# Kernel tuning notes

Measured on AMD Instinct MI355X. Metric: run time of the kernel, lower is better.

The kernel has to match this reference:

```python
import jax, jax.numpy as jnp
import numpy as np

V = 100000
E = 1600000
B, FIN, K, FOUT = 2, 32, 4, 32


def setup_inputs() -> dict:
    key = jax.random.key(0)
    k1, k2, k3, k4, k5, k6 = jax.random.split(key, 6)
    inputs = jax.random.normal(k1, (B, V, FIN), dtype=jnp.float32)
    lap_rows = jax.random.randint(k2, (E,), 0, V, dtype=jnp.int32)
    lap_cols = jax.random.randint(k3, (E,), 0, V, dtype=jnp.int32)
    # scale values so the Chebyshev recursion stays numerically tame
    lap_vals = jax.random.normal(k4, (E,), dtype=jnp.float32) * 0.1
    weight = jax.random.normal(k5, (FIN, K, FOUT), dtype=jnp.float32) * 0.05
    bias = jax.random.normal(k6, (FOUT,), dtype=jnp.float32)
    return {"inputs": inputs, "lap_rows": lap_rows, "lap_cols": lap_cols,
            "lap_vals": lap_vals, "weight": weight, "bias": bias}


def _spmm(rows, cols, vals, x):
    # sparse [V,V] @ dense [B,V,F] -> [B,V,F]
    gathered = jnp.take(x, cols, axis=1)            # [B,E,F]
    contrib = vals[None, :, None] * gathered        # [B,E,F]
    out = jax.ops.segment_sum(contrib.swapaxes(0, 1), rows, num_segments=V)  # [V,B,F]
    return out.swapaxes(0, 1)


def reference(inputs, lap_rows, lap_cols, lap_vals, weight, bias):
    k = weight.shape[1]
    x0 = inputs
    terms = [x0]
    if k > 1:
        x1 = _spmm(lap_rows, lap_cols, lap_vals, x0)
        terms.append(x1)
    for _ in range(2, k):
        x2 = 2.0 * _spmm(lap_rows, lap_cols, lap_vals, x1) - x0
        terms.append(x2)
        x0, x1 = x1, x2
    x = jnp.stack(terms, axis=-1)                   # [B,V,Fin,K]
    out = jnp.einsum('bvfk,fko->bvo', x, weight) + bias
    return out
```

## Files before the change

### kernel.cpp

```cpp
#include <hip/hip_runtime.h>
#include <hip/hip_bf16.h>

#define NV 100000
#define NE 1600000
#define NB 2
#define FIN 32
#define NK 4
#define FOUT 32

#define RPB 128
#define NBUCK ((NV + RPB - 1) / RPB)
#define SLAB 2816
#define CHUNK 8192
#define GCHUNK ((NE + CHUNK - 1) / CHUNK)
#define GCONV (((long)NV * 64 + 1023) / 1024)

typedef long long ll;


__global__ void scale_init_kernel(float* __restrict__ dst, const float* __restrict__ src,
                                  float alpha, int n) {
    int i = blockIdx.x * blockDim.x + threadIdx.x;
    if (i < n) dst[i] = alpha * src[i];
}

__global__ void spmm_scatter_kernel(float* __restrict__ y, const float* __restrict__ x,
                                    const int* __restrict__ rows, const int* __restrict__ cols,
                                    const float* __restrict__ vals, float scale) {
    long tid = (long)blockIdx.x * blockDim.x + threadIdx.x;
    int e = (int)(tid >> 5);
    int f = (int)(tid & 31);
    if (e >= NE) return;
    int r = rows[e];
    int c = cols[e];
    float v = scale * vals[e];
#pragma unroll
    for (int b = 0; b < NB; ++b) {
        float g = x[(long)b * NV * FIN + (long)c * FIN + f];
        atomicAdd(&y[(long)b * NV * FIN + (long)r * FIN + f], v * g);
    }
}

__global__ void term_gemm_kernel(float* __restrict__ out, const float* __restrict__ x,
                                 const float* __restrict__ weight, const float* __restrict__ bias,
                                 int k, int first) {
    __shared__ float Wl[FIN][FOUT];
    __shared__ float Xl[8][FIN];
    int tid = threadIdx.x;
    for (int i = tid; i < FIN * FOUT; i += 256) {
        int f = i >> 5, o = i & 31;
        Wl[f][o] = weight[f * (NK * FOUT) + k * FOUT + o];
    }
    long rbase = (long)blockIdx.x * 8;
    for (int i = tid; i < 8 * FIN; i += 256) {
        int rv = i >> 5, f = i & 31;
        Xl[rv][f] = x[(rbase + rv) * FIN + f];
    }
    __syncthreads();
    int rv = tid >> 5, o = tid & 31;
    float acc = 0.f;
#pragma unroll
    for (int f = 0; f < FIN; ++f) acc += Xl[rv][f] * Wl[f][o];
    long r = rbase + rv;
    if (first) out[r * FOUT + o] = acc + bias[o];
    else       out[r * FOUT + o] += acc;
}

__global__ __launch_bounds__(1024)
void convert_place_kernel(const int* __restrict__ rows, const int* __restrict__ cols,
                          const float* __restrict__ vals, int* __restrict__ gcursor,
                          ll* __restrict__ edges,
                          __hip_bfloat16* __restrict__ xb, const float* __restrict__ inputs) {
    if (blockIdx.x >= GCHUNK) {
        long i = (long)(blockIdx.x - GCHUNK) * 1024 + threadIdx.x;
        if (i < (long)NV * 64) {
            int lane = (int)(i & 63);
            long v = i >> 6;
            int b = lane >> 5, f = lane & 31;
            xb[i] = __float2bfloat16(inputs[(long)b * NV * FIN + v * FIN + f]);
        }
        return;
    }
    __shared__ int cnt[NBUCK];
    __shared__ int cur[NBUCK];
    for (int i = threadIdx.x; i < NBUCK; i += 1024) cnt[i] = 0;
    __syncthreads();
    long base = (long)blockIdx.x * CHUNK;
    int lim = (base + CHUNK <= NE) ? CHUNK : (int)(NE - base);
    for (int i = threadIdx.x; i < lim; i += 1024)
        atomicAdd(&cnt[rows[base + i] >> 7], 1);
    __syncthreads();
    for (int i = threadIdx.x; i < NBUCK; i += 1024)
        cur[i] = cnt[i] ? (i * SLAB + atomicAdd(&gcursor[i], cnt[i])) : 0;
    __syncthreads();
    if (lim == CHUNK) {
        int bb[8]; ll rec[8]; int pos[8];
#pragma unroll
        for (int u = 0; u < 8; ++u) {
            int i = threadIdx.x + u * 1024;
            int r = rows[base + i];
            bb[u] = r >> 7;
            unsigned int lo = ((unsigned int)cols[base + i]) | (((unsigned int)(r & 127)) << 17);
            unsigned int hi = __float_as_uint(vals[base + i]);
            rec[u] = (ll)lo | ((ll)hi << 32);
        }
#pragma unroll
        for (int u = 0; u < 8; ++u) pos[u] = atomicAdd(&cur[bb[u]], 1);
#pragma unroll
        for (int u = 0; u < 8; ++u)
            if (pos[u] < (bb[u] + 1) * SLAB) edges[pos[u]] = rec[u];
    } else {
        for (int i = threadIdx.x; i < lim; i += 1024) {
            int r = rows[base + i];
            int b = r >> 7;
            unsigned int lo = ((unsigned int)cols[base + i]) | (((unsigned int)(r & 127)) << 17);
            unsigned int hi = __float_as_uint(vals[base + i]);
            int pos = atomicAdd(&cur[b], 1);
            if (pos < (b + 1) * SLAB) edges[pos] = (ll)lo | ((ll)hi << 32);
        }
    }
}

__global__ __launch_bounds__(512)
void bucket_sort_kernel(ll* __restrict__ edges, const int* __restrict__ gcursor,
                        int* __restrict__ row_start, int* __restrict__ counts) {
    __shared__ ll recL[SLAB];
    __shared__ int rcnt[RPB];
    __shared__ int pcnt[RPB];
    __shared__ int rcur[RPB];
    __shared__ int ssc[RPB];
    int b = blockIdx.x;
    int base = b * SLAB;
    int n = gcursor[b];
    if (n > SLAB) n = SLAB;
    if (n < 0) n = 0;
    int t = threadIdx.x;
    if (t < RPB) rcnt[t] = 0;
    __syncthreads();
    {
        ll rc[4]; int lr[4]; bool vld[4];
#pragma unroll
        for (int u = 0; u < 4; ++u) {
            int i = t + u * 512;
            vld[u] = (i < n);
            if (vld[u]) { rc[u] = edges[base + i]; recL[i] = rc[u]; lr[u] = (int)((rc[u] >> 17) & 127); }
        }
#pragma unroll
        for (int u = 0; u < 4; ++u) if (vld[u]) atomicAdd(&rcnt[lr[u]], 1);
        for (int i = t + 2048; i < n; i += 512) {
            ll rec = edges[base + i];
            recL[i] = rec;
            atomicAdd(&rcnt[(int)((rec >> 17) & 127)], 1);
        }
    }
    __syncthreads();
    if (t < RPB) pcnt[t] = (rcnt[t] + 7) & ~7;
    __syncthreads();
    if (t < RPB) ssc[t] = pcnt[t];
    __syncthreads();
    for (int off = 1; off < RPB; off <<= 1) {
        int x = 0;
        if (t < RPB && t >= off) x = ssc[t - off];
        __syncthreads();
        if (t < RPB) ssc[t] += x;
        __syncthreads();
    }
    if (ssc[RPB - 1] > SLAB) {
        __syncthreads();
        if (t < RPB) { pcnt[t] = rcnt[t]; ssc[t] = rcnt[t]; }
        __syncthreads();
        for (int off = 1; off < RPB; off <<= 1) {
            int x = 0;
            if (t < RPB && t >= off) x = ssc[t - off];
            __syncthreads();
            if (t < RPB) ssc[t] += x;
            __syncthreads();
        }
    }
    __syncthreads();
    if (t < RPB) {
        int ex = ssc[t] - pcnt[t];
        rcur[t] = ex;
        int v = b * RPB + t;
        if (v < NV) { row_start[v] = base + ex; counts[v] = pcnt[t]; }
    }
    __syncthreads();
    {
        ll rc[4]; int lr[4]; int pos[4]; bool vld[4];
#pragma unroll
        for (int u = 0; u < 4; ++u) {
            int i = t + u * 512;
            vld[u] = (i < n);
            if (vld[u]) { rc[u] = recL[i]; lr[u] = (int)((rc[u] >> 17) & 127); }
        }
#pragma unroll
        for (int u = 0; u < 4; ++u) if (vld[u]) pos[u] = atomicAdd(&rcur[lr[u]], 1);
#pragma unroll
        for (int u = 0; u < 4; ++u) if (vld[u]) edges[base + pos[u]] = rc[u];
        for (int i = t + 2048; i < n; i += 512) {
            ll rec = recL[i];
            int pos = atomicAdd(&rcur[(int)((rec >> 17) & 127)], 1);
            edges[base + pos] = rec;
        }
    }
    __syncthreads();
    if (t < RPB) {
        int start = ssc[t] - pcnt[t];
        for (int i = rcnt[t]; i < pcnt[t]; ++i)
            edges[base + start + i] = 0;
    }
}

__global__ __launch_bounds__(256)
void spmm_gather_kernel(__hip_bfloat16* __restrict__ xnext, const __hip_bfloat16* __restrict__ xcur,
                        const __hip_bfloat16* __restrict__ xprev,
                        const int* __restrict__ row_start, const int* __restrict__ counts,
                        const ll* __restrict__ edges, float alpha, float beta) {
    int r = blockIdx.x * (blockDim.x >> 6) + (threadIdx.x >> 6);
    int lane = threadIdx.x & 63;
    int s = __builtin_amdgcn_readfirstlane(row_start[r]);
    int cnt = __builtin_amdgcn_readfirstlane(counts[r]);
    const ll* ep = edges + s;
    float acc = 0.f;
    int j = 0;
    for (; j + 16 <= cnt; j += 16) {
        ll e[16];
        unsigned int g[16];
#pragma unroll
        for (int u = 0; u < 16; ++u) e[u] = ep[j + u];
#pragma unroll
        for (int u = 0; u < 16; ++u)
            g[u] = ((const unsigned short*)xcur)[(long)(e[u] & 0x1FFFF) * 64 + lane];
#pragma unroll
        for (int u = 0; u < 16; ++u)
            acc = fmaf(__uint_as_float((unsigned int)((unsigned long long)e[u] >> 32)),
                       __uint_as_float((unsigned int)g[u] << 16), acc);
    }
    if (j + 8 <= cnt) {
        ll e[8];
        unsigned int g[8];
#pragma unroll
        for (int u = 0; u < 8; ++u) e[u] = ep[j + u];
#pragma unroll
        for (int u = 0; u < 8; ++u)
            g[u] = ((const unsigned short*)xcur)[(long)(e[u] & 0x1FFFF) * 64 + lane];
#pragma unroll
        for (int u = 0; u < 8; ++u)
            acc = fmaf(__uint_as_float((unsigned int)((unsigned long long)e[u] >> 32)),
                       __uint_as_float((unsigned int)g[u] << 16), acc);
        j += 8;
    }
    for (; j < cnt; ++j) {
        ll e0 = ep[j];
        unsigned int g0 = ((const unsigned short*)xcur)[(long)(e0 & 0x1FFFF) * 64 + lane];
        acc = fmaf(__uint_as_float((unsigned int)((unsigned long long)e0 >> 32)),
                   __uint_as_float(g0 << 16), acc);
    }
    long o = (long)r * 64 + lane;
    float res = alpha * acc;
    if (beta != 0.f) res += beta * __bfloat162float(xprev[o]);
    xnext[o] = __float2bfloat16(res);
}

__global__ __launch_bounds__(256)
void final_gemm_kernel(float* __restrict__ out,
                       const __hip_bfloat16* __restrict__ xb0,
                       const __hip_bfloat16* __restrict__ xb1,
                       const __hip_bfloat16* __restrict__ xb2,
                       const __hip_bfloat16* __restrict__ xb3,
                       const float* __restrict__ weight,
                       const float* __restrict__ bias) {
    int t = blockIdx.x * blockDim.x + threadIdx.x;
    if (t >= NV * NB) return;
    int oh = blockIdx.y * 16;
    int v = t >> 1, b = t & 1;
    float acc[16];
#pragma unroll
    for (int o = 0; o < 16; ++o) acc[o] = bias[oh + o];
    for (int k = 0; k < NK; ++k) {
        const __hip_bfloat16* xr = (k == 0) ? xb0 : (k == 1) ? xb1 : (k == 2) ? xb2 : xb3;
        const uint4* xp = (const uint4*)(xr + (long)v * 64 + b * 32);
        uint4 q0 = xp[0], q1 = xp[1], q2 = xp[2], q3 = xp[3];
        unsigned int qq[16] = {q0.x, q0.y, q0.z, q0.w, q1.x, q1.y, q1.z, q1.w,
                               q2.x, q2.y, q2.z, q2.w, q3.x, q3.y, q3.z, q3.w};
        const float* wk = weight + k * FOUT + oh;
#pragma unroll
        for (int i = 0; i < 16; ++i) {
            float xlo = __uint_as_float(qq[i] << 16);
            float xhi = __uint_as_float(qq[i] & 0xffff0000u);
            const float* w0 = wk + (2 * i) * (NK * FOUT);
            const float* w1 = wk + (2 * i + 1) * (NK * FOUT);
#pragma unroll
            for (int o = 0; o < 16; ++o) {
                acc[o] = fmaf(xlo, w0[o], acc[o]);
                acc[o] = fmaf(xhi, w1[o], acc[o]);
            }
        }
    }
    float* op = out + (long)b * NV * FOUT + (long)v * FOUT + oh;
#pragma unroll
    for (int o = 0; o < 16; ++o) op[o] = acc[o];
}

extern "C" void kernel_launch(void* const* d_in, const int* in_sizes, int n_in,
                              void* d_out, int out_size, void* d_ws, size_t ws_size,
                              hipStream_t stream) {
    const float* inputs = (const float*)d_in[0];
    const int*   rows   = (const int*)d_in[1];
    const int*   cols   = (const int*)d_in[2];
    const float* vals   = (const float*)d_in[3];
    const float* weight = (const float*)d_in[4];
    const float* bias   = (const float*)d_in[5];
    float* out = (float*)d_out;

    const long n = (long)NB * NV * FIN;
    const int gG = (NB * NV) / 8;
    const int gRow = NV / 4;
    const int gGemm = (NV * NB + 255) / 256;
    const int gFused = GCHUNK + (int)GCONV;

    int* gcursor   = (int*)d_ws;
    int* row_start = gcursor + 1024;
    int* counts    = row_start + NV;
    ll* edges      = (ll*)(counts + NV);
    size_t off = (size_t)((char*)(edges + (long)NBUCK * SLAB) - (char*)d_ws);
    off = (off + 255) & ~(size_t)255;
    __hip_bfloat16* xb0 = (__hip_bfloat16*)((char*)d_ws + off);
    __hip_bfloat16* xb1 = xb0 + (long)NV * 64;
    __hip_bfloat16* xb2 = xb1 + (long)NV * 64;
    __hip_bfloat16* xb3 = xb2 + (long)NV * 64;
    size_t need = off + 4 * (size_t)NV * 64 * sizeof(__hip_bfloat16);

    if (ws_size < need) {
        float* fA = (float*)d_ws;
        float* fB = fA + n;
        const int gNf = (int)((n + 255) / 256);
        const int gEf = (NE * 32 + 255) / 256;
        term_gemm_kernel<<<gG, 256, 0, stream>>>(out, inputs, weight, bias, 0, 1);
        scale_init_kernel<<<gNf, 256, 0, stream>>>(fA, inputs, 0.f, (int)n);
        spmm_scatter_kernel<<<gEf, 256, 0, stream>>>(fA, inputs, rows, cols, vals, 1.f);
        term_gemm_kernel<<<gG, 256, 0, stream>>>(out, fA, weight, bias, 1, 0);
        scale_init_kernel<<<gNf, 256, 0, stream>>>(fB, inputs, -1.f, (int)n);
        spmm_scatter_kernel<<<gEf, 256, 0, stream>>>(fB, fA, rows, cols, vals, 2.f);
        term_gemm_kernel<<<gG, 256, 0, stream>>>(out, fB, weight, bias, 2, 0);
        scale_init_kernel<<<gNf, 256, 0, stream>>>(fA, fA, -1.f, (int)n);
        spmm_scatter_kernel<<<gEf, 256, 0, stream>>>(fA, fB, rows, cols, vals, 2.f);
        term_gemm_kernel<<<gG, 256, 0, stream>>>(out, fA, weight, bias, 3, 0);
        return;
    }

    hipMemsetAsync(gcursor, 0, (size_t)NBUCK * sizeof(int), stream);
    convert_place_kernel<<<gFused, 1024, 0, stream>>>(rows, cols, vals, gcursor, edges,
                                                      xb0, inputs);
    bucket_sort_kernel<<<NBUCK, 512, 0, stream>>>(edges, gcursor, row_start, counts);

    spmm_gather_kernel<<<gRow, 256, 0, stream>>>(xb1, xb0, nullptr, row_start, counts,
                                                 edges, 1.f, 0.f);
    spmm_gather_kernel<<<gRow, 256, 0, stream>>>(xb2, xb1, xb0, row_start, counts,
                                                 edges, 2.f, -1.f);
    spmm_gather_kernel<<<gRow, 256, 0, stream>>>(xb3, xb2, xb1, row_start, counts,
                                                 edges, 2.f, -1.f);

    final_gemm_kernel<<<dim3(gGemm, 2), 256, 0, stream>>>(out, xb0, xb1, xb2, xb3,
                                                          weight, bias);
}
```

Measured before the change: 183.2 us.

## Fuse first SpMM gather into bucket sort kernel using LDS-resident sorted edges

The bucket sort kernel now keeps the row-sorted edge records in a second shared-memory array and, after sorting, computes the first Chebyshev SpMM (x1 = L x0) for its own 128 rows directly from LDS. The separate first spmm_gather launch goes away, along with its global reads of the edge list, row_start and counts. In exchange, LDS use per block doubles (two 2816-entry 64-bit arrays), which may lower occupancy. The gather runs with only 8 waves per block over 128 rows, so it has less latency hiding than the standalone kernel.

```diff
diff --git a/kernel.cpp b/kernel.cpp
--- a/kernel.cpp
+++ b/kernel.cpp
@@ -122,9 +122,12 @@
 }
 
 __global__ __launch_bounds__(512)
-void bucket_sort_kernel(ll* __restrict__ edges, const int* __restrict__ gcursor,
-                        int* __restrict__ row_start, int* __restrict__ counts) {
+void sort_gather_kernel(ll* __restrict__ edges, const int* __restrict__ gcursor,
+                        int* __restrict__ row_start, int* __restrict__ counts,
+                        __hip_bfloat16* __restrict__ xnext,
+                        const __hip_bfloat16* __restrict__ xcur) {
     __shared__ ll recL[SLAB];
+    __shared__ ll recS[SLAB];
     __shared__ int rcnt[RPB];
     __shared__ int pcnt[RPB];
     __shared__ int rcur[RPB];
@@ -196,18 +199,65 @@
 #pragma unroll
         for (int u = 0; u < 4; ++u) if (vld[u]) pos[u] = atomicAdd(&rcur[lr[u]], 1);
 #pragma unroll
-        for (int u = 0; u < 4; ++u) if (vld[u]) edges[base + pos[u]] = rc[u];
+        for (int u = 0; u < 4; ++u)
+            if (vld[u]) { recS[pos[u]] = rc[u]; edges[base + pos[u]] = rc[u]; }
         for (int i = t + 2048; i < n; i += 512) {
             ll rec = recL[i];
             int pos = atomicAdd(&rcur[(int)((rec >> 17) & 127)], 1);
+            recS[pos] = rec;
             edges[base + pos] = rec;
         }
     }
     __syncthreads();
     if (t < RPB) {
         int start = ssc[t] - pcnt[t];
-        for (int i = rcnt[t]; i < pcnt[t]; ++i)
+        for (int i = rcnt[t]; i < pcnt[t]; ++i) {
+            recS[start + i] = 0;
             edges[base + start + i] = 0;
+        }
+    }
+    __syncthreads();
+    int wid = t >> 6;
+    int lane = t & 63;
+    for (int lr = wid; lr < RPB; lr += 8) {
+        int row = b * RPB + lr;
+        if (row >= NV) break;
+        int st = ssc[lr] - pcnt[lr];
+        int cn = pcnt[lr];
+        float acc = 0.f;
+        int j = 0;
+        for (; j + 16 <= cn; j += 16) {
+            ll e[16]; unsigned int g[16];
+#pragma unroll
+            for (int u = 0; u < 16; ++u) e[u] = recS[st + j + u];
+#pragma unroll
+            for (int u = 0; u < 16; ++u)
+                g[u] = ((const unsigned short*)xcur)[(long)(e[u] & 0x1FFFF) * 64 + lane];
+#pragma unroll
+            for (int u = 0; u < 16; ++u)
+                acc = fmaf(__uint_as_float((unsigned int)((unsigned long long)e[u] >> 32)),
+                           __uint_as_float((unsigned int)g[u] << 16), acc);
+        }
+        if (j + 8 <= cn) {
+            ll e[8]; unsigned int g[8];
+#pragma unroll
+            for (int u = 0; u < 8; ++u) e[u] = recS[st + j + u];
+#pragma unroll
+            for (int u = 0; u < 8; ++u)
+                g[u] = ((const unsigned short*)xcur)[(long)(e[u] & 0x1FFFF) * 64 + lane];
+#pragma unroll
+            for (int u = 0; u < 8; ++u)
+                acc = fmaf(__uint_as_float((unsigned int)((unsigned long long)e[u] >> 32)),
+                           __uint_as_float((unsigned int)g[u] << 16), acc);
+            j += 8;
+        }
+        for (; j < cn; ++j) {
+            ll e0 = recS[st + j];
+            unsigned int g0 = ((const unsigned short*)xcur)[(long)(e0 & 0x1FFFF) * 64 + lane];
+            acc = fmaf(__uint_as_float((unsigned int)((unsigned long long)e0 >> 32)),
+                       __uint_as_float(g0 << 16), acc);
+        }
+        xnext[(long)row * 64 + lane] = __float2bfloat16(acc);
     }
 }
 
@@ -352,10 +402,8 @@
     hipMemsetAsync(gcursor, 0, (size_t)NBUCK * sizeof(int), stream);
     convert_place_kernel<<<gFused, 1024, 0, stream>>>(rows, cols, vals, gcursor, edges,
                                                       xb0, inputs);
-    bucket_sort_kernel<<<NBUCK, 512, 0, stream>>>(edges, gcursor, row_start, counts);
-
-    spmm_gather_kernel<<<gRow, 256, 0, stream>>>(xb1, xb0, nullptr, row_start, counts,
-                                                 edges, 1.f, 0.f);
+    sort_gather_kernel<<<NBUCK, 512, 0, stream>>>(edges, gcursor, row_start, counts,
+                                                  xb1, xb0);
     spmm_gather_kernel<<<gRow, 256, 0, stream>>>(xb2, xb1, xb0, row_start, counts,
                                                  edges, 2.f, -1.f);
     spmm_gather_kernel<<<gRow, 256, 0, stream>>>(xb3, xb2, xb1, row_start, counts,
```

Result: slower. 188.6 us (+2.9%).
